# Kernel tuning notes

Measured on AMD Instinct MI355X. Metric: run time of the kernel, lower is better.

## Reference

```python
import jax, jax.numpy as jnp
import numpy as np

HIDDEN = 1024
N_HEADS = 16
HEAD_DIM = HIDDEN // N_HEADS  # 64
SCALE = HEAD_DIM ** -0.5
B, QL, KVL = 2, 2048, 4096


def setup_inputs() -> dict:
    key = jax.random.key(0)
    ks = jax.random.split(key, 7)
    s = 0.02
    return {
        "query_states": jax.random.normal(ks[0], (B, QL, HIDDEN), jnp.float32),
        "key_states": jax.random.normal(ks[1], (B, KVL, HIDDEN), jnp.float32),
        "value_states": jax.random.normal(ks[2], (B, KVL, HIDDEN), jnp.float32),
        # torch nn.Linear weights: shape [out, in], applied as x @ W.T
        "Wq": jax.random.normal(ks[3], (HIDDEN, HIDDEN), jnp.float32) * s,
        "Wk": jax.random.normal(ks[4], (HIDDEN, HIDDEN), jnp.float32) * s,
        "Wv": jax.random.normal(ks[5], (HIDDEN, HIDDEN), jnp.float32) * s,
        "Wo": jax.random.normal(ks[6], (HIDDEN, HIDDEN), jnp.float32) * s,
    }


def reference(query_states, key_states, value_states, Wq, Wk, Wv, Wo):
    b, ql, _ = query_states.shape
    kvl = key_states.shape[1]
    # projections (torch Linear: x @ W.T)
    q = query_states @ Wq.T  # [b, ql, H]
    k = key_states @ Wk.T    # [b, kvl, H]
    v = value_states @ Wv.T  # [b, kvl, H]
    # split heads -> [b, h, s, d]
    q = q.reshape(b, ql, N_HEADS, HEAD_DIM).transpose(0, 2, 1, 3)
    k = k.reshape(b, kvl, N_HEADS, HEAD_DIM).transpose(0, 2, 1, 3)
    v = v.reshape(b, kvl, N_HEADS, HEAD_DIM).transpose(0, 2, 1, 3)
    # scores [b, h, ql, kvl]
    scores = jnp.einsum("bhqd,bhkd->bhqk", q, k) * SCALE
    attn = jax.nn.softmax(scores, axis=-1)
    out = jnp.einsum("bhqk,bhkd->bhqd", attn, v)  # [b, h, ql, d]
    out = out.transpose(0, 2, 1, 3).reshape(b, ql, HIDDEN)
    return out @ Wo.T
```

## Files before the change

### kernel.cpp

```cpp
#include <hip/hip_runtime.h>

#define HID   1024
#define NH    16
#define HD    64
#define QL    2048
#define KVL   4096
#define NB    2
#define QSCALE 0.180336880111120426f

typedef short s8v  __attribute__((ext_vector_type(8)));
typedef short s4v  __attribute__((ext_vector_type(4)));
typedef float f4v  __attribute__((ext_vector_type(4)));

__device__ __forceinline__ unsigned short f2bf(float f) {
  unsigned int u = __builtin_bit_cast(unsigned int, f);
  u += 0x7FFFu + ((u >> 16) & 1u);
  return (unsigned short)(u >> 16);
}

__device__ __forceinline__ float fexp2(float x) {
#if __has_builtin(__builtin_amdgcn_exp2f)
  return __builtin_amdgcn_exp2f(x);
#else
  return exp2f(x);
#endif
}

__global__ __launch_bounds__(256)
void cast_all(const float* __restrict__ q, const float* __restrict__ k,
              const float* __restrict__ v, const float* __restrict__ wq,
              const float* __restrict__ wk, const float* __restrict__ wv,
              const float* __restrict__ wo, unsigned short* __restrict__ dst) {
  size_t c = (size_t)blockIdx.x * 256 + threadIdx.x;
  const float* src; size_t lc; float sc = 1.0f;
  if (c < 524288)       { src = q;  lc = c; }
  else if (c < 1572864) { src = k;  lc = c - 524288; }
  else if (c < 2621440) { src = v;  lc = c - 1572864; }
  else if (c < 2752512) { src = wq; lc = c - 2621440; sc = QSCALE; }
  else if (c < 2883584) { src = wk; lc = c - 2752512; }
  else if (c < 3014656) { src = wv; lc = c - 2883584; }
  else                  { src = wo; lc = c - 3014656; }
  const float4* p = (const float4*)(src + lc * 8);
  float4 a = p[0], b = p[1];
  union { s8v v8; unsigned short h[8]; } u;
  u.h[0] = f2bf(a.x * sc); u.h[1] = f2bf(a.y * sc);
  u.h[2] = f2bf(a.z * sc); u.h[3] = f2bf(a.w * sc);
  u.h[4] = f2bf(b.x * sc); u.h[5] = f2bf(b.y * sc);
  u.h[6] = f2bf(b.z * sc); u.h[7] = f2bf(b.w * sc);
  *(s8v*)(dst + c * 8) = u.v8;
}

typedef const __attribute__((address_space(1))) unsigned int* gas_t;
typedef __attribute__((address_space(3))) unsigned int*       las_t;

__device__ __forceinline__ void gl_lds16(const unsigned short* g, unsigned short* l) {
  __builtin_amdgcn_global_load_lds((gas_t)(const void*)g, (las_t)(void*)l, 16, 0, 0);
}

template <bool OUT_BF16>
__device__ __forceinline__ void gemm_body(const unsigned short* __restrict__ A,
                                          const unsigned short* __restrict__ B,
                                          void* __restrict__ Cv, int N, int K,
                                          int bx, int by,
                                          unsigned short* As, unsigned short* Bs) {
  const int tid  = threadIdx.x;
  const int wave = tid >> 6, lane = tid & 63;
  const int wm = wave >> 1, wn = wave & 1;
  const int quad = lane >> 4, l15 = lane & 15;
  const int row0 = by * 128;
  const int col0 = bx * 128;
  const int srow = lane >> 2;
  const int scol = (lane & 3) * 8;

  f4v acc[4][4] = {};

  for (int k0 = 0; k0 < K; k0 += 32) {
    __syncthreads();
#pragma unroll
    for (int cc = 0; cc < 2; cc++) {
      int c = wave + cc * 4;
      gl_lds16(A + (size_t)(row0 + c * 16 + srow) * K + k0 + scol, &As[c * 512]);
      gl_lds16(B + (size_t)(col0 + c * 16 + srow) * K + k0 + scol, &Bs[c * 512]);
    }
    __syncthreads();

    s8v af[4], bf[4];
#pragma unroll
    for (int i = 0; i < 4; i++)
      af[i] = *(const s8v*)&As[(wm * 64 + i * 16 + l15) * 32 + quad * 8];
#pragma unroll
    for (int j = 0; j < 4; j++)
      bf[j] = *(const s8v*)&Bs[(wn * 64 + j * 16 + l15) * 32 + quad * 8];
#pragma unroll
    for (int i = 0; i < 4; i++)
#pragma unroll
      for (int j = 0; j < 4; j++)
        acc[i][j] = __builtin_amdgcn_mfma_f32_16x16x32_bf16(af[i], bf[j],
                                                            acc[i][j], 0, 0, 0);
  }

#pragma unroll
  for (int i = 0; i < 4; i++) {
#pragma unroll
    for (int j = 0; j < 4; j++) {
      int r = row0 + wm * 64 + i * 16 + quad * 4;
      int c = col0 + wn * 64 + j * 16 + l15;
#pragma unroll
      for (int reg = 0; reg < 4; reg++) {
        float v = acc[i][j][reg];
        if constexpr (OUT_BF16)
          ((unsigned short*)Cv)[(size_t)(r + reg) * N + c] = f2bf(v);
        else
          ((float*)Cv)[(size_t)(r + reg) * N + c] = v;
      }
    }
  }
}

__global__ __launch_bounds__(256, 2)
void proj_fused(const unsigned short* __restrict__ qc, const unsigned short* __restrict__ kc,
                const unsigned short* __restrict__ vc, const unsigned short* __restrict__ wqc,
                const unsigned short* __restrict__ wkc, const unsigned short* __restrict__ wvc,
                unsigned short* __restrict__ qp, unsigned short* __restrict__ kp,
                unsigned short* __restrict__ vpt) {
  __shared__ unsigned short As[128 * 32];
  __shared__ unsigned short Bs[128 * 32];
  int bid = blockIdx.x;
  if (bid < 256) {
    gemm_body<true>(qc, wqc, qp, HID, HID, bid & 7, bid >> 3, As, Bs);
  } else if (bid < 768) {
    int l = bid - 256;
    gemm_body<true>(kc, wkc, kp, HID, HID, l & 7, l >> 3, As, Bs);
  } else {
    int l = bid - 768;
    int b = l >> 8, r = l & 255;
    gemm_body<true>(wvc, vc + (size_t)b * KVL * HID,
                    vpt + (size_t)b * HID * KVL, KVL, HID, r & 31, r >> 5, As, Bs);
  }
}

__global__ __launch_bounds__(256, 2)
void o_gemm(const unsigned short* __restrict__ ao, const unsigned short* __restrict__ woc,
            float* __restrict__ out) {
  __shared__ unsigned short As[128 * 32];
  __shared__ unsigned short Bs[128 * 32];
  int bid = blockIdx.x;
  gemm_body<false>(ao, woc, out, HID, HID, bid & 7, bid >> 3, As, Bs);
}

#define LDSK 40

template <typename T>
__device__ __forceinline__ void stage_tile(unsigned short* dst, const T* src,
                                           int ld, int tid, float sc) {
#pragma unroll
  for (int rep = 0; rep < 2; rep++) {
    int s = rep * 256 + tid;
    int row = s >> 2;
    int cs  = (s & 3) * 8;
    const T* p = src + (size_t)row * ld + cs;
    s8v val;
    if constexpr (sizeof(T) == 4) {
      float4 f0 = *(const float4*)p;
      float4 f1 = *(const float4*)(p + 4);
      union { s8v v; unsigned short h[8]; } u;
      u.h[0] = f2bf(f0.x * sc); u.h[1] = f2bf(f0.y * sc);
      u.h[2] = f2bf(f0.z * sc); u.h[3] = f2bf(f0.w * sc);
      u.h[4] = f2bf(f1.x * sc); u.h[5] = f2bf(f1.y * sc);
      u.h[6] = f2bf(f1.z * sc); u.h[7] = f2bf(f1.w * sc);
      val = u.v;
    } else {
      val = *(const s8v*)p;
    }
    *(s8v*)&dst[row * LDSK + cs] = val;
  }
}

template <typename TA, typename TB, bool OUT_BF16>
__global__ __launch_bounds__(256)
void gemm_conv(const TA* __restrict__ A, const TB* __restrict__ B,
               void* __restrict__ Cv, int M, int N, int K, float bscale,
               long long bz, long long cz) {
  __shared__ unsigned short As[128 * LDSK];
  __shared__ unsigned short Bs[128 * LDSK];
  const TB* Bp = B + (size_t)blockIdx.z * (size_t)bz;
  const int tid  = threadIdx.x;
  const int wave = tid >> 6, lane = tid & 63;
  const int wm = wave >> 1, wn = wave & 1;
  const int quad = lane >> 4, l15 = lane & 15;
  const int row0 = blockIdx.y * 128;
  const int col0 = blockIdx.x * 128;

  f4v acc[4][4] = {};

  for (int k0 = 0; k0 < K; k0 += 32) {
    __syncthreads();
    stage_tile(As, A + (size_t)row0 * K + k0, K, tid, 1.0f);
    stage_tile(Bs, Bp + (size_t)col0 * K + k0, K, tid, bscale);
    __syncthreads();

    s8v af[4], bf[4];
#pragma unroll
    for (int i = 0; i < 4; i++)
      af[i] = *(const s8v*)&As[(wm * 64 + i * 16 + l15) * LDSK + quad * 8];
#pragma unroll
    for (int j = 0; j < 4; j++)
      bf[j] = *(const s8v*)&Bs[(wn * 64 + j * 16 + l15) * LDSK + quad * 8];
#pragma unroll
    for (int i = 0; i < 4; i++)
#pragma unroll
      for (int j = 0; j < 4; j++)
        acc[i][j] = __builtin_amdgcn_mfma_f32_16x16x32_bf16(af[i], bf[j],
                                                            acc[i][j], 0, 0, 0);
  }

  char* Cp = (char*)Cv + (size_t)blockIdx.z * (size_t)cz * (OUT_BF16 ? 2 : 4);
#pragma unroll
  for (int i = 0; i < 4; i++) {
#pragma unroll
    for (int j = 0; j < 4; j++) {
      int r = row0 + wm * 64 + i * 16 + quad * 4;
      int c = col0 + wn * 64 + j * 16 + l15;
#pragma unroll
      for (int reg = 0; reg < 4; reg++) {
        float v = acc[i][j][reg];
        if constexpr (OUT_BF16)
          ((unsigned short*)Cp)[(size_t)(r + reg) * N + c] = f2bf(v);
        else
          ((float*)Cp)[(size_t)(r + reg) * N + c] = v;
      }
    }
  }
}

#define AST 72

__global__ __launch_bounds__(256, 1)
void attn4(const unsigned short* __restrict__ qp,
           const unsigned short* __restrict__ kp,
           const unsigned short* __restrict__ vpt,
           unsigned short* __restrict__ ao) {
  __shared__ unsigned short Ks[3][64 * 64];
  __shared__ unsigned short Vt[3][64 * 64];
  __shared__ unsigned short Pt[4][64 * AST];

  const int bid  = blockIdx.x;
  const int qb   = bid & 7;
  const int h    = (bid >> 3) & 15;
  const int b    = bid >> 7;
  const int tid  = threadIdx.x;
  const int wave = tid >> 6, lane = tid & 63;
  const int quad = lane >> 4, l15 = lane & 15;
  const int q0   = qb * 256 + wave * 64;

  const unsigned short* kbase = kp + (size_t)b * KVL * HID + h * HD;
  const unsigned short* vbase = vpt + (size_t)(b * NH + h) * HD * KVL;

  int prow[2], pcol[2], pbase[2];
#pragma unroll
  for (int i = 0; i < 2; i++) {
    int p = (i * 4 + wave) * 64 + lane;
    prow[i]  = p >> 3;
    pcol[i]  = ((p & 7) ^ (prow[i] & 7)) * 8;
    pbase[i] = (i * 4 + wave) * 512;
  }

  s8v qf[4][2];
#pragma unroll
  for (int nt = 0; nt < 4; nt++) {
    const size_t qrow = (size_t)(b * QL + q0 + nt * 16 + l15) * HID + h * HD;
#pragma unroll
    for (int ks = 0; ks < 2; ks++)
      qf[nt][ks] = *(const s8v*)(qp + qrow + ks * 32 + quad * 8);
  }

  float lrun[4] = {0.f, 0.f, 0.f, 0.f};
  f4v oacc[4][4] = {};

#define STAGE_KV(KT, BI)                                                        \
  {                                                                             \
    const unsigned short* kb = kbase + (size_t)((KT) * 64) * HID;               \
    const unsigned short* vb = vbase + (KT) * 64;                               \
    _Pragma("unroll")                                                           \
    for (int i = 0; i < 2; i++) {                                               \
      gl_lds16(kb + (size_t)prow[i] * HID + pcol[i], &Ks[BI][pbase[i]]);        \
      gl_lds16(vb + (size_t)prow[i] * KVL + pcol[i], &Vt[BI][pbase[i]]);        \
    }                                                                           \
  }

  constexpr int NT = KVL / 64;
  STAGE_KV(0, 0);
  STAGE_KV(1, 1);
  __syncthreads();

  for (int kt = 0; kt < NT; kt++) {
    const int cur = kt % 3;
    if (kt + 2 < NT) STAGE_KV(kt + 2, (kt + 2) % 3);

    f4v sacc[4][4] = {};
#pragma unroll
    for (int ks = 0; ks < 2; ks++)
#pragma unroll
      for (int mt = 0; mt < 4; mt++) {
        int row = mt * 16 + l15;
        int xc  = ((ks * 4 + quad) ^ (row & 7)) * 8;
        s8v kf = *(const s8v*)&Ks[cur][row * 64 + xc];
#pragma unroll
        for (int nt = 0; nt < 4; nt++)
          sacc[mt][nt] = __builtin_amdgcn_mfma_f32_16x16x32_bf16(kf, qf[nt][ks],
                                                                 sacc[mt][nt], 0, 0, 0);
      }

#pragma unroll
    for (int nt = 0; nt < 4; nt++) {
      float rs = 0.f;
#pragma unroll
      for (int mt = 0; mt < 4; mt++) {
        float p0 = fexp2(sacc[mt][nt][0]);
        float p1 = fexp2(sacc[mt][nt][1]);
        float p2 = fexp2(sacc[mt][nt][2]);
        float p3 = fexp2(sacc[mt][nt][3]);
        rs += (p0 + p1) + (p2 + p3);
        union { s4v v4; unsigned short hh[4]; } pk;
        pk.hh[0] = f2bf(p0); pk.hh[1] = f2bf(p1);
        pk.hh[2] = f2bf(p2); pk.hh[3] = f2bf(p3);
        *(s4v*)&Pt[wave][(nt * 16 + l15) * AST + mt * 16 + quad * 4] = pk.v4;
      }
      rs += __shfl_xor(rs, 16, 64);
      rs += __shfl_xor(rs, 32, 64);
      lrun[nt] += rs;
    }

#pragma unroll
    for (int ch = 0; ch < 2; ch++) {
      s8v vf[4];
#pragma unroll
      for (int dt = 0; dt < 4; dt++) {
        int row = dt * 16 + l15;
        int xc  = ((ch * 4 + quad) ^ (row & 7)) * 8;
        vf[dt] = *(const s8v*)&Vt[cur][row * 64 + xc];
      }
#pragma unroll
      for (int qt = 0; qt < 4; qt++) {
        s8v pf = *(const s8v*)&Pt[wave][(qt * 16 + l15) * AST + ch * 32 + quad * 8];
#pragma unroll
        for (int dt = 0; dt < 4; dt++)
          oacc[qt][dt] = __builtin_amdgcn_mfma_f32_16x16x32_bf16(pf, vf[dt],
                                                                 oacc[qt][dt], 0, 0, 0);
      }
    }

    __syncthreads();
  }

#pragma unroll
  for (int qt = 0; qt < 4; qt++) {
    float li = 1.0f / lrun[qt];
    float lr[4];
#pragma unroll
    for (int r = 0; r < 4; r++)
      lr[r] = __shfl(li, (lane & 48) + quad * 4 + r, 64);
#pragma unroll
    for (int dt = 0; dt < 4; dt++)
#pragma unroll
      for (int r = 0; r < 4; r++) {
        int qq = q0 + qt * 16 + quad * 4 + r;
        int cc = h * HD + dt * 16 + l15;
        ao[(size_t)(b * QL + qq) * HID + cc] = f2bf(oacc[qt][dt][r] * lr[r]);
      }
  }
#undef STAGE_KV
}

extern "C" void kernel_launch(void* const* d_in, const int* in_sizes, int n_in,
                              void* d_out, int out_size, void* d_ws, size_t ws_size,
                              hipStream_t stream) {
  const float* q  = (const float*)d_in[0];
  const float* k  = (const float*)d_in[1];
  const float* v  = (const float*)d_in[2];
  const float* Wq = (const float*)d_in[3];
  const float* Wk = (const float*)d_in[4];
  const float* Wv = (const float*)d_in[5];
  const float* Wo = (const float*)d_in[6];
  float* out = (float*)d_out;
  char* ws = (char*)d_ws;
  dim3 blk(256);

  const long long MB = 1024 * 1024;
  if (ws_size >= (size_t)88 * MB) {
    unsigned short* qc  = (unsigned short*)(ws);
    unsigned short* kc  = (unsigned short*)(ws + 8 * MB);
    unsigned short* vc  = (unsigned short*)(ws + 24 * MB);
    unsigned short* wqc = (unsigned short*)(ws + 40 * MB);
    unsigned short* wkc = (unsigned short*)(ws + 42 * MB);
    unsigned short* wvc = (unsigned short*)(ws + 44 * MB);
    unsigned short* woc = (unsigned short*)(ws + 46 * MB);
    unsigned short* qp  = (unsigned short*)(ws + 48 * MB);
    unsigned short* kp  = (unsigned short*)(ws + 56 * MB);
    unsigned short* vpt = (unsigned short*)(ws + 72 * MB);
    unsigned short* ao  = (unsigned short*)(ws);

    cast_all<<<12288, blk, 0, stream>>>(q, k, v, Wq, Wk, Wv, Wo, (unsigned short*)ws);
    proj_fused<<<1280, blk, 0, stream>>>(qc, kc, vc, wqc, wkc, wvc, qp, kp, vpt);
    attn4<<<256, blk, 0, stream>>>(qp, kp, vpt, ao);
    o_gemm<<<256, blk, 0, stream>>>(ao, woc, out);
  } else {
    unsigned short* qp  = (unsigned short*)(ws);
    unsigned short* kp  = (unsigned short*)(ws + 8 * MB);
    unsigned short* vpt = (unsigned short*)(ws + 24 * MB);
    unsigned short* ao  = (unsigned short*)(ws + 40 * MB);

    gemm_conv<float, float, true><<<dim3(8, 32), blk, 0, stream>>>(q, Wq, qp, NB * QL, HID, HID, QSCALE, 0, 0);
    gemm_conv<float, float, true><<<dim3(8, 64), blk, 0, stream>>>(k, Wk, kp, NB * KVL, HID, HID, 1.0f, 0, 0);
    gemm_conv<float, float, true><<<dim3(32, 8, 2), blk, 0, stream>>>(Wv, v, vpt, HID, KVL, HID, 1.0f,
                                                                      (long long)KVL * HID, (long long)HID * KVL);
    attn4<<<256, blk, 0, stream>>>(qp, kp, vpt, ao);
    gemm_conv<unsigned short, float, false><<<dim3(8, 32), blk, 0, stream>>>(ao, Wo, out, NB * QL, HID, HID, 1.0f, 0, 0);
  }
}
```

Baseline: 344.8 us.

## Double-buffer GEMM LDS tiles and split attention into smaller query blocks

The projection and output GEMMs now double-buffer their LDS tiles. The next K-slice is prefetched while the current one is multiplied, which drops one barrier per iteration. The attention kernel now handles 128 queries per block (32 per wave) instead of 256, with two K/V buffers instead of three. It launches 512 blocks with two blocks per CU allowed, to raise occupancy and fill the GPU better. The cost is more K/V reloads across blocks and a shallower prefetch depth.

```diff
diff --git a/kernel.cpp b/kernel.cpp
--- a/kernel.cpp
+++ b/kernel.cpp
@@ -62,7 +62,8 @@
                                           const unsigned short* __restrict__ B,
                                           void* __restrict__ Cv, int N, int K,
                                           int bx, int by,
-                                          unsigned short* As, unsigned short* Bs) {
+                                          unsigned short (*As)[128 * 32],
+                                          unsigned short (*Bs)[128 * 32]) {
   const int tid  = threadIdx.x;
   const int wave = tid >> 6, lane = tid & 63;
   const int wm = wave >> 1, wn = wave & 1;
@@ -74,30 +75,42 @@
 
   f4v acc[4][4] = {};
 
-  for (int k0 = 0; k0 < K; k0 += 32) {
-    __syncthreads();
-#pragma unroll
-    for (int cc = 0; cc < 2; cc++) {
-      int c = wave + cc * 4;
-      gl_lds16(A + (size_t)(row0 + c * 16 + srow) * K + k0 + scol, &As[c * 512]);
-      gl_lds16(B + (size_t)(col0 + c * 16 + srow) * K + k0 + scol, &Bs[c * 512]);
-    }
-    __syncthreads();
+#define G_STAGE(KI, BI)                                                         \
+  {                                                                             \
+    _Pragma("unroll")                                                           \
+    for (int cc = 0; cc < 2; cc++) {                                            \
+      int c = wave + cc * 4;                                                    \
+      gl_lds16(A + (size_t)(row0 + c * 16 + srow) * K + (KI) * 32 + scol,       \
+               &As[BI][c * 512]);                                               \
+      gl_lds16(B + (size_t)(col0 + c * 16 + srow) * K + (KI) * 32 + scol,       \
+               &Bs[BI][c * 512]);                                               \
+    }                                                                           \
+  }
+
+  const int nk = K >> 5;
+  G_STAGE(0, 0);
+  __syncthreads();
+
+  for (int ki = 0; ki < nk; ki++) {
+    const int cur = ki & 1;
+    if (ki + 1 < nk) G_STAGE(ki + 1, 1 - cur);
 
     s8v af[4], bf[4];
 #pragma unroll
     for (int i = 0; i < 4; i++)
-      af[i] = *(const s8v*)&As[(wm * 64 + i * 16 + l15) * 32 + quad * 8];
+      af[i] = *(const s8v*)&As[cur][(wm * 64 + i * 16 + l15) * 32 + quad * 8];
 #pragma unroll
     for (int j = 0; j < 4; j++)
-      bf[j] = *(const s8v*)&Bs[(wn * 64 + j * 16 + l15) * 32 + quad * 8];
+      bf[j] = *(const s8v*)&Bs[cur][(wn * 64 + j * 16 + l15) * 32 + quad * 8];
 #pragma unroll
     for (int i = 0; i < 4; i++)
 #pragma unroll
       for (int j = 0; j < 4; j++)
         acc[i][j] = __builtin_amdgcn_mfma_f32_16x16x32_bf16(af[i], bf[j],
                                                             acc[i][j], 0, 0, 0);
-  }
+    __syncthreads();
+  }
+#undef G_STAGE
 
 #pragma unroll
   for (int i = 0; i < 4; i++) {
@@ -123,8 +136,8 @@
                 const unsigned short* __restrict__ wkc, const unsigned short* __restrict__ wvc,
                 unsigned short* __restrict__ qp, unsigned short* __restrict__ kp,
                 unsigned short* __restrict__ vpt) {
-  __shared__ unsigned short As[128 * 32];
-  __shared__ unsigned short Bs[128 * 32];
+  __shared__ unsigned short As[2][128 * 32];
+  __shared__ unsigned short Bs[2][128 * 32];
   int bid = blockIdx.x;
   if (bid < 256) {
     gemm_body<true>(qc, wqc, qp, HID, HID, bid & 7, bid >> 3, As, Bs);
@@ -142,8 +155,8 @@
 __global__ __launch_bounds__(256, 2)
 void o_gemm(const unsigned short* __restrict__ ao, const unsigned short* __restrict__ woc,
             float* __restrict__ out) {
-  __shared__ unsigned short As[128 * 32];
-  __shared__ unsigned short Bs[128 * 32];
+  __shared__ unsigned short As[2][128 * 32];
+  __shared__ unsigned short Bs[2][128 * 32];
   int bid = blockIdx.x;
   gemm_body<false>(ao, woc, out, HID, HID, bid & 7, bid >> 3, As, Bs);
 }
@@ -235,23 +248,23 @@
 
 #define AST 72
 
-__global__ __launch_bounds__(256, 1)
-void attn4(const unsigned short* __restrict__ qp,
+__global__ __launch_bounds__(256, 2)
+void attn5(const unsigned short* __restrict__ qp,
            const unsigned short* __restrict__ kp,
            const unsigned short* __restrict__ vpt,
            unsigned short* __restrict__ ao) {
-  __shared__ unsigned short Ks[3][64 * 64];
-  __shared__ unsigned short Vt[3][64 * 64];
-  __shared__ unsigned short Pt[4][64 * AST];
+  __shared__ unsigned short Ks[2][64 * 64];
+  __shared__ unsigned short Vt[2][64 * 64];
+  __shared__ unsigned short Pt[4][32 * AST];
 
   const int bid  = blockIdx.x;
-  const int qb   = bid & 7;
-  const int h    = (bid >> 3) & 15;
-  const int b    = bid >> 7;
+  const int qb   = bid & 15;
+  const int h    = (bid >> 4) & 15;
+  const int b    = bid >> 8;
   const int tid  = threadIdx.x;
   const int wave = tid >> 6, lane = tid & 63;
   const int quad = lane >> 4, l15 = lane & 15;
-  const int q0   = qb * 256 + wave * 64;
+  const int q0   = qb * 128 + wave * 32;
 
   const unsigned short* kbase = kp + (size_t)b * KVL * HID + h * HD;
   const unsigned short* vbase = vpt + (size_t)(b * NH + h) * HD * KVL;
@@ -265,17 +278,17 @@
     pbase[i] = (i * 4 + wave) * 512;
   }
 
-  s8v qf[4][2];
-#pragma unroll
-  for (int nt = 0; nt < 4; nt++) {
-    const size_t qrow = (size_t)(b * QL + q0 + nt * 16 + l15) * HID + h * HD;
+  s8v qf[2][2];
+#pragma unroll
+  for (int qt = 0; qt < 2; qt++) {
+    const size_t qrow = (size_t)(b * QL + q0 + qt * 16 + l15) * HID + h * HD;
 #pragma unroll
     for (int ks = 0; ks < 2; ks++)
-      qf[nt][ks] = *(const s8v*)(qp + qrow + ks * 32 + quad * 8);
-  }
-
-  float lrun[4] = {0.f, 0.f, 0.f, 0.f};
-  f4v oacc[4][4] = {};
+      qf[qt][ks] = *(const s8v*)(qp + qrow + ks * 32 + quad * 8);
+  }
+
+  float lrun[2] = {0.f, 0.f};
+  f4v oacc[2][4] = {};
 
 #define STAGE_KV(KT, BI)                                                        \
   {                                                                             \
@@ -290,14 +303,13 @@
 
   constexpr int NT = KVL / 64;
   STAGE_KV(0, 0);
-  STAGE_KV(1, 1);
   __syncthreads();
 
   for (int kt = 0; kt < NT; kt++) {
-    const int cur = kt % 3;
-    if (kt + 2 < NT) STAGE_KV(kt + 2, (kt + 2) % 3);
-
-    f4v sacc[4][4] = {};
+    const int cur = kt & 1;
+    if (kt + 1 < NT) STAGE_KV(kt + 1, 1 - cur);
+
+    f4v sacc[2][4] = {};
 #pragma unroll
     for (int ks = 0; ks < 2; ks++)
 #pragma unroll
@@ -306,29 +318,29 @@
         int xc  = ((ks * 4 + quad) ^ (row & 7)) * 8;
         s8v kf = *(const s8v*)&Ks[cur][row * 64 + xc];
 #pragma unroll
-        for (int nt = 0; nt < 4; nt++)
-          sacc[mt][nt] = __builtin_amdgcn_mfma_f32_16x16x32_bf16(kf, qf[nt][ks],
-                                                                 sacc[mt][nt], 0, 0, 0);
-      }
-
-#pragma unroll
-    for (int nt = 0; nt < 4; nt++) {
+        for (int qt = 0; qt < 2; qt++)
+          sacc[qt][mt] = __builtin_amdgcn_mfma_f32_16x16x32_bf16(kf, qf[qt][ks],
+                                                                 sacc[qt][mt], 0, 0, 0);
+      }
+
+#pragma unroll
+    for (int qt = 0; qt < 2; qt++) {
       float rs = 0.f;
 #pragma unroll
       for (int mt = 0; mt < 4; mt++) {
-        float p0 = fexp2(sacc[mt][nt][0]);
-        float p1 = fexp2(sacc[mt][nt][1]);
-        float p2 = fexp2(sacc[mt][nt][2]);
-        float p3 = fexp2(sacc[mt][nt][3]);
+        float p0 = fexp2(sacc[qt][mt][0]);
+        float p1 = fexp2(sacc[qt][mt][1]);
+        float p2 = fexp2(sacc[qt][mt][2]);
+        float p3 = fexp2(sacc[qt][mt][3]);
         rs += (p0 + p1) + (p2 + p3);
         union { s4v v4; unsigned short hh[4]; } pk;
         pk.hh[0] = f2bf(p0); pk.hh[1] = f2bf(p1);
         pk.hh[2] = f2bf(p2); pk.hh[3] = f2bf(p3);
-        *(s4v*)&Pt[wave][(nt * 16 + l15) * AST + mt * 16 + quad * 4] = pk.v4;
+        *(s4v*)&Pt[wave][(qt * 16 + l15) * AST + mt * 16 + quad * 4] = pk.v4;
       }
       rs += __shfl_xor(rs, 16, 64);
       rs += __shfl_xor(rs, 32, 64);
-      lrun[nt] += rs;
+      lrun[qt] += rs;
     }
 
 #pragma unroll
@@ -341,7 +353,7 @@
         vf[dt] = *(const s8v*)&Vt[cur][row * 64 + xc];
       }
 #pragma unroll
-      for (int qt = 0; qt < 4; qt++) {
+      for (int qt = 0; qt < 2; qt++) {
         s8v pf = *(const s8v*)&Pt[wave][(qt * 16 + l15) * AST + ch * 32 + quad * 8];
 #pragma unroll
         for (int dt = 0; dt < 4; dt++)
@@ -352,9 +364,10 @@
 
     __syncthreads();
   }
-
-#pragma unroll
-  for (int qt = 0; qt < 4; qt++) {
+#undef STAGE_KV
+
+#pragma unroll
+  for (int qt = 0; qt < 2; qt++) {
     float li = 1.0f / lrun[qt];
     float lr[4];
 #pragma unroll
@@ -369,7 +382,6 @@
         ao[(size_t)(b * QL + qq) * HID + cc] = f2bf(oacc[qt][dt][r] * lr[r]);
       }
   }
-#undef STAGE_KV
 }
 
 extern "C" void kernel_launch(void* const* d_in, const int* in_sizes, int n_in,
@@ -402,7 +414,7 @@
 
     cast_all<<<12288, blk, 0, stream>>>(q, k, v, Wq, Wk, Wv, Wo, (unsigned short*)ws);
     proj_fused<<<1280, blk, 0, stream>>>(qc, kc, vc, wqc, wkc, wvc, qp, kp, vpt);
-    attn4<<<256, blk, 0, stream>>>(qp, kp, vpt, ao);
+    attn5<<<512, blk, 0, stream>>>(qp, kp, vpt, ao);
     o_gemm<<<256, blk, 0, stream>>>(ao, woc, out);
   } else {
     unsigned short* qp  = (unsigned short*)(ws);
@@ -414,7 +426,7 @@
     gemm_conv<float, float, true><<<dim3(8, 64), blk, 0, stream>>>(k, Wk, kp, NB * KVL, HID, HID, 1.0f, 0, 0);
     gemm_conv<float, float, true><<<dim3(32, 8, 2), blk, 0, stream>>>(Wv, v, vpt, HID, KVL, HID, 1.0f,
                                                                       (long long)KVL * HID, (long long)HID * KVL);
-    attn4<<<256, blk, 0, stream>>>(qp, kp, vpt, ao);
+    attn5<<<512, blk, 0, stream>>>(qp, kp, vpt, ao);
     gemm_conv<unsigned short, float, false><<<dim3(8, 32), blk, 0, stream>>>(ao, Wo, out, NB * QL, HID, HID, 1.0f, 0, 0);
   }
 }
```

Result: faster. 335.1 us (-2.8%).
